# Performance work log

Measured on AMD Instinct MI355X. Metric: run time of the kernel, lower is better.

## Reference

```python
import jax, jax.numpy as jnp
import numpy as np

HEADS = 2
BN_EPS = 1e-5


def _axial_self_attn(x, Wq, Wkv, Wout, bout):
    # x: (b, s, t, c) -- attend along t (the axial sequence dim)
    b, s, t, c = x.shape
    dh = c // HEADS
    q = (x @ Wq).reshape(b, s, t, HEADS, dh)
    k, v = jnp.split(x @ Wkv, 2, axis=-1)  # matches torch .chunk(2, dim=-1)
    k = k.reshape(b, s, t, HEADS, dh)
    v = v.reshape(b, s, t, HEADS, dh)
    dots = jnp.einsum('bsind,bsjnd->bsnij', q, k) * (dh ** -0.5)
    attn = jax.nn.softmax(dots, axis=-1)
    out = jnp.einsum('bsnij,bsjnd->bsind', attn, v).reshape(b, s, t, c)
    return out @ Wout + bout


def setup_inputs() -> dict:
    key = jax.random.key(0)
    ks = jax.random.split(key, 8)
    B, C, H, W = 8, 128, 256, 256
    E = 2 * C
    sd = 0.05
    return {
        'x': jax.random.normal(ks[0], (B, C, H, W), jnp.float32),
        'Wq_h': jax.random.normal(ks[1], (C, C), jnp.float32) * sd,
        'Wkv_h': jax.random.normal(ks[2], (C, 2 * C), jnp.float32) * sd,
        'Wout_h': jax.random.normal(ks[3], (C, C), jnp.float32) * sd,
        'bout_h': jnp.zeros((C,), jnp.float32),
        'Wq_w': jax.random.normal(ks[4], (C, C), jnp.float32) * sd,
        'Wkv_w': jax.random.normal(ks[5], (C, 2 * C), jnp.float32) * sd,
        'Wout_w': jax.random.normal(ks[6], (C, C), jnp.float32) * sd,
        'bout_w': jnp.zeros((C,), jnp.float32),
        'conv_w': jax.random.normal(ks[7], (E, E), jnp.float32) * sd,  # (in, out); torch conv weight[o,i,0,0].T
        'gamma': jnp.ones((E,), jnp.float32),
        'beta': jnp.zeros((E,), jnp.float32),
    }


def reference(x, Wq_h, Wkv_h, Wout_h, bout_h, Wq_w, Wkv_w, Wout_w, bout_w, conv_w, gamma, beta):
    B, C, H, W = x.shape
    # MaxPool2d(2)
    xp = x.reshape(B, C, H // 2, 2, W // 2, 2).max(axis=(3, 5))  # (B,C,H2,W2)
    xc = jnp.transpose(xp, (0, 2, 3, 1))  # (B,H2,W2,C) channels-last
    # AxialAttention, sum_axial_out=True: height-axis attn + width-axis attn
    a_h = _axial_self_attn(jnp.transpose(xc, (0, 2, 1, 3)), Wq_h, Wkv_h, Wout_h, bout_h)
    a_h = jnp.transpose(a_h, (0, 2, 1, 3))
    a_w = _axial_self_attn(xc, Wq_w, Wkv_w, Wout_w, bout_w)
    a = jax.nn.relu(a_h + a_w)
    # cat((x_attn, x), dim=channel) then conv1x1 -> relu -> BatchNorm (batch stats)
    y = jnp.concatenate([a, xc], axis=-1) @ conv_w  # (B,H2,W2,2C)
    y = jax.nn.relu(y)
    mean = y.mean(axis=(0, 1, 2))
    var = y.var(axis=(0, 1, 2))
    y = (y - mean) * jax.lax.rsqrt(var + BN_EPS) * gamma + beta
    return jnp.transpose(y, (0, 3, 1, 2))  # back to NCHW
```

## Files before the change

kernel.cpp:

```cpp
#include <hip/hip_runtime.h>


typedef short v8s __attribute__((ext_vector_type(8)));
typedef short v4s __attribute__((ext_vector_type(4)));
typedef float v4f __attribute__((ext_vector_type(4)));

#define LSA 136
#define LSC 264
#define LSP 130

static __device__ __forceinline__ short f2bf(float f){
  unsigned u = __builtin_bit_cast(unsigned, f);
  u = (u + 0x7FFFu + ((u >> 16) & 1u)) >> 16;
  return (short)u;
}
static __device__ __forceinline__ float bf2f(short s){
  unsigned u = ((unsigned)(unsigned short)s) << 16;
  return __builtin_bit_cast(float, u);
}

__global__ void prep_kernel(const float* __restrict__ Wq_h, const float* __restrict__ Wkv_h,
                            const float* __restrict__ Wout_h, const float* __restrict__ Wq_w,
                            const float* __restrict__ Wkv_w, const float* __restrict__ Wout_w,
                            const float* __restrict__ conv_w, short* __restrict__ wt,
                            float* __restrict__ stats){
  int idx = blockIdx.x * 256 + threadIdx.x;
  if (idx < 8192) stats[idx] = 0.0f;
  const float* src; int K, O, base;
  if      (idx <  16384){ base = 0;      K=128; O=128; src=Wq_h;  }
  else if (idx <  49152){ base = 16384;  K=128; O=256; src=Wkv_h; }
  else if (idx <  65536){ base = 49152;  K=128; O=128; src=Wout_h;}
  else if (idx <  81920){ base = 65536;  K=128; O=128; src=Wq_w;  }
  else if (idx < 114688){ base = 81920;  K=128; O=256; src=Wkv_w; }
  else if (idx < 131072){ base = 114688; K=128; O=128; src=Wout_w;}
  else                  { base = 131072; K=256; O=256; src=conv_w;}
  int local = idx - base;
  int o = local / K, i = local - o * K;
  wt[idx] = f2bf(src[i * O + o]);
}

__global__ __launch_bounds__(256, 4)
void pool_kernel(const float* __restrict__ x, short* __restrict__ xph,
                 short* __restrict__ xpw){
  __shared__ short t_[128*LSP];
  int bx = blockIdx.x;
  int b = bx >> 7, i = bx & 127;
  int tid = (int)threadIdx.x;
  int j  = tid & 127;
  int ch = tid >> 7;
  for (int rep = 0; rep < 64; ++rep){
    int c = rep*2 + ch;
    const float* p0 = x + (((b*128 + c)*256 + 2*i)*256 + 2*j);
    float2 a  = *(const float2*)p0;
    float2 bb = *(const float2*)(p0 + 256);
    t_[j*LSP + c] = f2bf(fmaxf(fmaxf(a.x, a.y), fmaxf(bb.x, bb.y)));
  }
  __syncthreads();
  int obase_h = ((b*128 + i)*128)*128;
  for (int rep = 0; rep < 8; ++rep){
    int idx = rep*256 + tid;
    int row = idx >> 4, seg = idx & 15;
    v8s v = *(const v8s*)(&t_[row*LSP + seg*8]);
    *(v8s*)(xph + obase_h + row*128 + seg*8) = v;
    *(v8s*)(xpw + ((b*128 + row)*128 + i)*128 + seg*8) = v;
  }
}

__global__ __launch_bounds__(512, 2)
void attn_kernel(const short* __restrict__ xp_hw, const short* __restrict__ xp_wh,
                 const short* __restrict__ wt,
                 const float* __restrict__ bout_h, const float* __restrict__ bout_w,
                 short* __restrict__ ah, short* __restrict__ aw){
  __shared__ short A[128*LSA];
  __shared__ short WB[128*LSA];

  const int bx = blockIdx.x;
  const int dir = bx & 1;
  const int sb = bx >> 1;
  const int b = sb >> 7, s = sb & 127;
  const int tid = (int)threadIdx.x;
  const int w = tid >> 6;
  const int lane = tid & 63;
  const int l15 = lane & 15, l4 = lane >> 4;

  const short* Wq   = wt + dir*65536;
  const short* Wk   = Wq + 16384;
  const short* Wv   = Wq + 32768;
  const short* Wout = Wq + 49152;
  const float* bsrc = dir ? bout_w : bout_h;
  const short* xsrc = dir ? xp_hw : xp_wh;
  short*       ao   = dir ? aw : ah;

  const int xbase = ((b*128 + s)*128 + (16*w + l15))*128;
  v8s av[4];
  #pragma unroll
  for (int kk = 0; kk < 4; ++kk)
    av[kk] = *(const v8s*)(xsrc + xbase + kk*32 + l4*8);
  v8s wq_r[4], wk_r[4], wv_r[4], wo_r[4];
  #pragma unroll
  for (int r = 0; r < 4; ++r){
    int idx = (r*512 + tid) * 8;
    wq_r[r] = *(const v8s*)(Wq   + idx);
    wk_r[r] = *(const v8s*)(Wk   + idx);
    wv_r[r] = *(const v8s*)(Wv   + idx);
    wo_r[r] = *(const v8s*)(Wout + idx);
  }

#define STAGE_R(RG)                                                      \
  { _Pragma("unroll")                                                    \
    for (int r_ = 0; r_ < 4; ++r_){                                      \
      int idx_ = (r_*512 + tid) * 8;                                     \
      int oc_ = idx_ >> 7, ic_ = idx_ & 127;                             \
      *(v8s*)(&WB[oc_*LSA + ic_]) = RG[r_];                              \
    } }

  STAGE_R(wq_r);
  __syncthreads();

  #pragma unroll
  for (int tc = 0; tc < 8; ++tc){
    v4f d = {0.f,0.f,0.f,0.f};
    #pragma unroll
    for (int kk = 0; kk < 4; ++kk){
      v8s bf = *(const v8s*)(&WB[(tc*16 + l15)*LSA + kk*32 + l4*8]);
      d = __builtin_amdgcn_mfma_f32_16x16x32_bf16(av[kk], bf, d, 0, 0, 0);
    }
    #pragma unroll
    for (int r = 0; r < 4; ++r)
      A[(16*w + 4*l4 + r)*LSA + 16*tc + l15] = f2bf(d[r]);
  }
  v8s bq[2][2];
  #pragma unroll
  for (int h = 0; h < 2; ++h)
    #pragma unroll
    for (int kk = 0; kk < 2; ++kk)
      bq[h][kk] = *(const v8s*)(&A[(16*w + l15)*LSA + h*64 + kk*32 + l4*8]);
  __syncthreads();

  STAGE_R(wk_r);
  __syncthreads();

  #pragma unroll
  for (int tc = 0; tc < 8; ++tc){
    v4f d = {0.f,0.f,0.f,0.f};
    #pragma unroll
    for (int kk = 0; kk < 4; ++kk){
      v8s bf = *(const v8s*)(&WB[(tc*16 + l15)*LSA + kk*32 + l4*8]);
      d = __builtin_amdgcn_mfma_f32_16x16x32_bf16(av[kk], bf, d, 0, 0, 0);
    }
    #pragma unroll
    for (int r = 0; r < 4; ++r)
      A[(16*w + 4*l4 + r)*LSA + 16*tc + l15] = f2bf(d[r]);
  }
  __syncthreads();

  STAGE_R(wv_r);

  v4s pk[2][8];
  #pragma unroll
  for (int h = 0; h < 2; ++h){
    v4f st[8];
    #pragma unroll
    for (int jt = 0; jt < 8; ++jt){
      v4f d = {0.f,0.f,0.f,0.f};
      #pragma unroll
      for (int kk = 0; kk < 2; ++kk){
        v8s ak = *(const v8s*)(&A[(16*jt + l15)*LSA + h*64 + kk*32 + l4*8]);
        d = __builtin_amdgcn_mfma_f32_16x16x32_bf16(ak, bq[h][kk], d, 0, 0, 0);
      }
      st[jt] = d;
    }
    float mx = -1e30f;
    #pragma unroll
    for (int jt = 0; jt < 8; ++jt)
      #pragma unroll
      for (int r = 0; r < 4; ++r) mx = fmaxf(mx, st[jt][r]);
    mx = fmaxf(mx, __shfl_xor(mx, 16));
    mx = fmaxf(mx, __shfl_xor(mx, 32));
    float sm = 0.f;
    #pragma unroll
    for (int jt = 0; jt < 8; ++jt)
      #pragma unroll
      for (int r = 0; r < 4; ++r){
        float e = __expf((st[jt][r] - mx) * 0.125f);
        st[jt][r] = e; sm += e;
      }
    sm += __shfl_xor(sm, 16);
    sm += __shfl_xor(sm, 32);
    float inv = 1.0f / sm;
    #pragma unroll
    for (int jt = 0; jt < 8; ++jt)
      #pragma unroll
      for (int r = 0; r < 4; ++r) pk[h][jt][r] = f2bf(st[jt][r] * inv);
  }
  __syncthreads();

  v8s pa[2][4];
  #pragma unroll
  for (int h = 0; h < 2; ++h){
    #pragma unroll
    for (int jt = 0; jt < 8; ++jt)
      *(v4s*)(&A[(16*w + l15)*LSA + 16*jt + 4*l4]) = pk[h][jt];
    #pragma unroll
    for (int kk = 0; kk < 4; ++kk)
      pa[h][kk] = *(const v8s*)(&A[(16*w + l15)*LSA + kk*32 + l4*8]);
  }
  __syncthreads();

  #pragma unroll
  for (int tc = 0; tc < 8; ++tc){
    v4f d = {0.f,0.f,0.f,0.f};
    #pragma unroll
    for (int kk = 0; kk < 4; ++kk){
      v8s bf = *(const v8s*)(&WB[(tc*16 + l15)*LSA + kk*32 + l4*8]);
      d = __builtin_amdgcn_mfma_f32_16x16x32_bf16(av[kk], bf, d, 0, 0, 0);
    }
    v4s pkv;
    #pragma unroll
    for (int r = 0; r < 4; ++r) pkv[r] = f2bf(d[r]);
    *(v4s*)(&A[(16*tc + l15)*LSA + 16*w + 4*l4]) = pkv;
  }
  __syncthreads();

  STAGE_R(wo_r);

  v4f ot[2][4];
  #pragma unroll
  for (int h = 0; h < 2; ++h)
    #pragma unroll
    for (int tc = 0; tc < 4; ++tc){
      v4f d = {0.f,0.f,0.f,0.f};
      #pragma unroll
      for (int kk = 0; kk < 4; ++kk){
        v8s vf = *(const v8s*)(&A[(64*h + 16*tc + l15)*LSA + kk*32 + l4*8]);
        d = __builtin_amdgcn_mfma_f32_16x16x32_bf16(vf, pa[h][kk], d, 0, 0, 0);
      }
      ot[h][tc] = d;
    }
  __syncthreads();

  #pragma unroll
  for (int h = 0; h < 2; ++h)
    #pragma unroll
    for (int tc = 0; tc < 4; ++tc){
      v4s pko;
      #pragma unroll
      for (int r = 0; r < 4; ++r) pko[r] = f2bf(ot[h][tc][r]);
      *(v4s*)(&A[(16*w + l15)*LSA + 64*h + 16*tc + 4*l4]) = pko;
    }
  v8s ob[4];
  #pragma unroll
  for (int kk = 0; kk < 4; ++kk)
    ob[kk] = *(const v8s*)(&A[(16*w + l15)*LSA + kk*32 + l4*8]);
  #pragma unroll
  for (int tc = 0; tc < 8; ++tc){
    v4f d = {0.f,0.f,0.f,0.f};
    #pragma unroll
    for (int kk = 0; kk < 4; ++kk){
      v8s awf = *(const v8s*)(&WB[(tc*16 + l15)*LSA + kk*32 + l4*8]);
      d = __builtin_amdgcn_mfma_f32_16x16x32_bf16(awf, ob[kk], d, 0, 0, 0);
    }
    v4f bias = *(const v4f*)(bsrc + 16*tc + 4*l4);
    v4s z;
    #pragma unroll
    for (int r = 0; r < 4; ++r) z[r] = f2bf(d[r] + bias[r]);
    *(v4s*)(&A[(16*w + l15)*LSA + 16*tc + 4*l4]) = z;
  }
  __syncthreads();

  int obase = ((b*128 + s)*128)*128;
  #pragma unroll
  for (int r = 0; r < 4; ++r){
    int idx = (r*512 + tid) * 8;
    int t = idx >> 7, c = idx & 127;
    *(v8s*)(ao + obase + t*128 + c) = *(const v8s*)(&A[t*LSA + c]);
  }
#undef STAGE_R
}

__global__ __launch_bounds__(512, 2)
void conv_kernel(const short* __restrict__ ah, const short* __restrict__ aw,
                 const short* __restrict__ xp, const short* __restrict__ wt,
                 short* __restrict__ yb, float* __restrict__ stats){
  __shared__ short cats[128*LSC];
  __shared__ float lsum[256];
  __shared__ float lsq[256];
  const short* convT = wt + 131072;
  int bx = blockIdx.x;
  int b = bx >> 7, ii = bx & 127;
  int tid = (int)threadIdx.x;
  int wv = tid >> 6, lane = tid & 63, l15 = lane & 15, l4 = lane >> 4;
  if (tid < 256){ lsum[tid] = 0.f; lsq[tid] = 0.f; }

  v8s wf[2][8];
  #pragma unroll
  for (int x = 0; x < 2; ++x)
    #pragma unroll
    for (int kk = 0; kk < 8; ++kk)
      wf[x][kk] = *(const v8s*)(convT + (((wv + 8*x)*16 + l15)*256) + kk*32 + l4*8);

  for (int r = 0; r < 4; ++r){
    int idx = (r*512 + tid) * 8;
    int t = idx >> 7, c = idx & 127;
    v8s hv = *(const v8s*)(ah + ((b*128 + t)*128 + ii)*128 + c);
    v8s wv_ = *(const v8s*)(aw + ((b*128 + ii)*128 + t)*128 + c);
    v8s o;
    #pragma unroll
    for (int k = 0; k < 8; ++k)
      o[k] = f2bf(fmaxf(bf2f(hv[k]) + bf2f(wv_[k]), 0.f));
    *(v8s*)(&cats[t*LSC + c]) = o;
    *(v8s*)(&cats[t*LSC + 128 + c]) =
        *(const v8s*)(xp + ((b*128 + ii)*128 + t)*128 + c);
  }
  __syncthreads();

  v4s ypk[2][8];
  float s1[2] = {0.f,0.f}, s2[2] = {0.f,0.f};
  #pragma unroll
  for (int tt = 0; tt < 8; ++tt){
    v4f d0 = {0.f,0.f,0.f,0.f}, d1 = {0.f,0.f,0.f,0.f};
    #pragma unroll
    for (int kk = 0; kk < 8; ++kk){
      v8s af = *(const v8s*)(&cats[(16*tt + l15)*LSC + kk*32 + l4*8]);
      d0 = __builtin_amdgcn_mfma_f32_16x16x32_bf16(af, wf[0][kk], d0, 0, 0, 0);
      d1 = __builtin_amdgcn_mfma_f32_16x16x32_bf16(af, wf[1][kk], d1, 0, 0, 0);
    }
    #pragma unroll
    for (int r = 0; r < 4; ++r){
      float y0 = fmaxf(d0[r], 0.f), y1 = fmaxf(d1[r], 0.f);
      ypk[0][tt][r] = f2bf(y0); ypk[1][tt][r] = f2bf(y1);
      s1[0] += y0; s2[0] += y0*y0;
      s1[1] += y1; s2[1] += y1*y1;
    }
  }
  #pragma unroll
  for (int x = 0; x < 2; ++x){
    s1[x] += __shfl_xor(s1[x], 16); s1[x] += __shfl_xor(s1[x], 32);
    s2[x] += __shfl_xor(s2[x], 16); s2[x] += __shfl_xor(s2[x], 32);
  }
  if (l4 == 0){
    #pragma unroll
    for (int x = 0; x < 2; ++x){
      int e = (wv + 8*x)*16 + l15;
      atomicAdd(&lsum[e], s1[x]);
      atomicAdd(&lsq[e],  s2[x]);
    }
  }
  __syncthreads();
  #pragma unroll
  for (int x = 0; x < 2; ++x)
    #pragma unroll
    for (int tt = 0; tt < 8; ++tt)
      *(v4s*)(&cats[((wv + 8*x)*16 + l15)*132 + 16*tt + 4*l4]) = ypk[x][tt];
  __syncthreads();
  for (int r = 0; r < 8; ++r){
    int idx = (r*512 + tid) * 8;
    int e = idx >> 7, j = idx & 127;
    *(v8s*)(yb + ((b*256 + e)*128 + ii)*128 + j) = *(const v8s*)(&cats[e*132 + j]);
  }
  if (tid < 256){
    int c = bx & 15;
    atomicAdd(&stats[c*512 + tid],       lsum[tid]);
    atomicAdd(&stats[c*512 + 256 + tid], lsq[tid]);
  }
}

__global__ void bn_kernel(const short* __restrict__ yb, float* __restrict__ out,
                          const float* __restrict__ stats,
                          const float* __restrict__ gamma, const float* __restrict__ beta){
  const float invn = 1.0f / 131072.0f;
  int bx = blockIdx.x;
  int e = bx & 255;
  float s1 = 0.f, s2 = 0.f;
  #pragma unroll
  for (int c = 0; c < 16; ++c){
    s1 += stats[c*512 + e];
    s2 += stats[c*512 + 256 + e];
  }
  float m   = s1 * invn;
  float var = s2 * invn - m * m;
  float sc  = gamma[e] * rsqrtf(var + 1e-5f);
  float sh  = beta[e] - m * sc;
  int base = bx * 16384;
  int tid = (int)threadIdx.x;
  for (int rep = 0; rep < 8; ++rep){
    int idx = base + (rep*256 + tid)*8;
    v8s yv = *(const v8s*)(yb + idx);
    v4f o1, o2;
    #pragma unroll
    for (int r = 0; r < 4; ++r){
      o1[r] = bf2f(yv[r])   * sc + sh;
      o2[r] = bf2f(yv[4+r]) * sc + sh;
    }
    *(v4f*)(out + idx)     = o1;
    *(v4f*)(out + idx + 4) = o2;
  }
}

extern "C" void kernel_launch(void* const* d_in, const int* in_sizes, int n_in,
                              void* d_out, int out_size, void* d_ws, size_t ws_size,
                              hipStream_t stream){
  const float* x      = (const float*)d_in[0];
  const float* Wq_h   = (const float*)d_in[1];
  const float* Wkv_h  = (const float*)d_in[2];
  const float* Wout_h = (const float*)d_in[3];
  const float* bout_h = (const float*)d_in[4];
  const float* Wq_w   = (const float*)d_in[5];
  const float* Wkv_w  = (const float*)d_in[6];
  const float* Wout_w = (const float*)d_in[7];
  const float* bout_w = (const float*)d_in[8];
  const float* conv_w = (const float*)d_in[9];
  const float* gamma  = (const float*)d_in[10];
  const float* beta   = (const float*)d_in[11];
  float* out = (float*)d_out;

  char* ws = (char*)d_ws;
  short* xp_hw = (short*)(ws);
  short* xp_wh = (short*)(ws +  33554432);
  short* ah    = (short*)(ws +  67108864);
  short* aw    = (short*)(ws + 100663296);
  short* yb    = (short*)(ws + 134217728);
  short* wt    = (short*)(ws + 201326592);
  float* stats = (float*)(ws + 201719808);

  prep_kernel<<<768, 256, 0, stream>>>(Wq_h, Wkv_h, Wout_h, Wq_w, Wkv_w, Wout_w,
                                       conv_w, wt, stats);
  pool_kernel<<<1024, 256, 0, stream>>>(x, xp_hw, xp_wh);
  attn_kernel<<<2048, 512, 0, stream>>>(xp_hw, xp_wh, wt, bout_h, bout_w, ah, aw);
  conv_kernel<<<1024, 512, 0, stream>>>(ah, aw, xp_hw, wt, yb, stats);
  bn_kernel<<<2048, 256, 0, stream>>>(yb, out, stats, gamma, beta);
}
```

Baseline: 283.4 us.

## Cut attention kernel register pressure and vectorize pooling loads

The pooling kernel now reads four floats per load, producing two pooled outputs per thread, so it issues fewer, wider global loads. The attention kernel stops holding all four weight matrices in registers and loads each one directly from global memory into LDS just before it is used. The projection GEMMs are re-tiled so each wave computes a 32-row by 64-column block instead of 16 rows by 128 columns. Together with launch bounds raised from 2 to 4 blocks per CU, this aims to lower register use and raise occupancy. The cost is that weight-load latency is now exposed at each staging step rather than prefetched.

```diff
diff --git a/kernel.cpp b/kernel.cpp
--- a/kernel.cpp
+++ b/kernel.cpp
@@ -4,6 +4,7 @@
 typedef short v8s __attribute__((ext_vector_type(8)));
 typedef short v4s __attribute__((ext_vector_type(4)));
 typedef float v4f __attribute__((ext_vector_type(4)));
+typedef float v4flt __attribute__((ext_vector_type(4)));
 
 #define LSA 136
 #define LSC 264
@@ -46,14 +47,15 @@
   int bx = blockIdx.x;
   int b = bx >> 7, i = bx & 127;
   int tid = (int)threadIdx.x;
-  int j  = tid & 127;
-  int ch = tid >> 7;
-  for (int rep = 0; rep < 64; ++rep){
-    int c = rep*2 + ch;
-    const float* p0 = x + (((b*128 + c)*256 + 2*i)*256 + 2*j);
-    float2 a  = *(const float2*)p0;
-    float2 bb = *(const float2*)(p0 + 256);
-    t_[j*LSP + c] = f2bf(fmaxf(fmaxf(a.x, a.y), fmaxf(bb.x, bb.y)));
+  int j2 = tid & 63;
+  int cq = tid >> 6;
+  for (int rep = 0; rep < 32; ++rep){
+    int c = cq*32 + rep;
+    const float* p0 = x + (((b*128 + c)*256 + 2*i)*256 + 4*j2);
+    v4flt a  = *(const v4flt*)p0;
+    v4flt bb = *(const v4flt*)(p0 + 256);
+    t_[(2*j2)*LSP + c]   = f2bf(fmaxf(fmaxf(a[0], a[1]), fmaxf(bb[0], bb[1])));
+    t_[(2*j2+1)*LSP + c] = f2bf(fmaxf(fmaxf(a[2], a[3]), fmaxf(bb[2], bb[3])));
   }
   __syncthreads();
   int obase_h = ((b*128 + i)*128)*128;
@@ -66,7 +68,7 @@
   }
 }
 
-__global__ __launch_bounds__(512, 2)
+__global__ __launch_bounds__(512, 4)
 void attn_kernel(const short* __restrict__ xp_hw, const short* __restrict__ xp_wh,
                  const short* __restrict__ wt,
                  const float* __restrict__ bout_h, const float* __restrict__ bout_w,
@@ -80,6 +82,8 @@
   const int b = sb >> 7, s = sb & 127;
   const int tid = (int)threadIdx.x;
   const int w = tid >> 6;
+  const int m = w >> 1;
+  const int p = w & 1;
   const int lane = tid & 63;
   const int l15 = lane & 15, l4 = lane >> 4;
 
@@ -91,70 +95,59 @@
   const short* xsrc = dir ? xp_hw : xp_wh;
   short*       ao   = dir ? aw : ah;
 
-  const int xbase = ((b*128 + s)*128 + (16*w + l15))*128;
-  v8s av[4];
-  #pragma unroll
-  for (int kk = 0; kk < 4; ++kk)
-    av[kk] = *(const v8s*)(xsrc + xbase + kk*32 + l4*8);
-  v8s wq_r[4], wk_r[4], wv_r[4], wo_r[4];
-  #pragma unroll
-  for (int r = 0; r < 4; ++r){
-    int idx = (r*512 + tid) * 8;
-    wq_r[r] = *(const v8s*)(Wq   + idx);
-    wk_r[r] = *(const v8s*)(Wk   + idx);
-    wv_r[r] = *(const v8s*)(Wv   + idx);
-    wo_r[r] = *(const v8s*)(Wout + idx);
-  }
-
-#define STAGE_R(RG)                                                      \
+  v8s av[2][4];
+  #pragma unroll
+  for (int ti = 0; ti < 2; ++ti){
+    int xbase = ((b*128 + s)*128 + (32*m + 16*ti + l15))*128;
+    #pragma unroll
+    for (int kk = 0; kk < 4; ++kk)
+      av[ti][kk] = *(const v8s*)(xsrc + xbase + kk*32 + l4*8);
+  }
+
+#define STAGE_W(SRC)                                                     \
   { _Pragma("unroll")                                                    \
     for (int r_ = 0; r_ < 4; ++r_){                                      \
       int idx_ = (r_*512 + tid) * 8;                                     \
       int oc_ = idx_ >> 7, ic_ = idx_ & 127;                             \
-      *(v8s*)(&WB[oc_*LSA + ic_]) = RG[r_];                              \
+      *(v8s*)(&WB[oc_*LSA + ic_]) = *(const v8s*)((SRC) + idx_);         \
     } }
 
-  STAGE_R(wq_r);
-  __syncthreads();
-
-  #pragma unroll
-  for (int tc = 0; tc < 8; ++tc){
-    v4f d = {0.f,0.f,0.f,0.f};
-    #pragma unroll
-    for (int kk = 0; kk < 4; ++kk){
-      v8s bf = *(const v8s*)(&WB[(tc*16 + l15)*LSA + kk*32 + l4*8]);
-      d = __builtin_amdgcn_mfma_f32_16x16x32_bf16(av[kk], bf, d, 0, 0, 0);
-    }
-    #pragma unroll
-    for (int r = 0; r < 4; ++r)
-      A[(16*w + 4*l4 + r)*LSA + 16*tc + l15] = f2bf(d[r]);
-  }
+#define WGEMM_TO_A()                                                     \
+  { _Pragma("unroll")                                                    \
+    for (int ti = 0; ti < 2; ++ti){                                      \
+      _Pragma("unroll")                                                  \
+      for (int tc = 0; tc < 4; ++tc){                                    \
+        int ocb = 64*p + 16*tc;                                          \
+        v4f d = {0.f,0.f,0.f,0.f};                                       \
+        _Pragma("unroll")                                                \
+        for (int kk = 0; kk < 4; ++kk){                                  \
+          v8s bf = *(const v8s*)(&WB[(ocb + l15)*LSA + kk*32 + l4*8]);   \
+          d = __builtin_amdgcn_mfma_f32_16x16x32_bf16(av[ti][kk], bf, d, 0, 0, 0); \
+        }                                                                \
+        _Pragma("unroll")                                                \
+        for (int r = 0; r < 4; ++r)                                      \
+          A[(32*m + 16*ti + 4*l4 + r)*LSA + ocb + l15] = f2bf(d[r]);     \
+      } } }
+
+  STAGE_W(Wq);
+  __syncthreads();
+
+  WGEMM_TO_A();
+  __syncthreads();
+
   v8s bq[2][2];
   #pragma unroll
   for (int h = 0; h < 2; ++h)
     #pragma unroll
     for (int kk = 0; kk < 2; ++kk)
       bq[h][kk] = *(const v8s*)(&A[(16*w + l15)*LSA + h*64 + kk*32 + l4*8]);
-  __syncthreads();
-
-  STAGE_R(wk_r);
-  __syncthreads();
-
-  #pragma unroll
-  for (int tc = 0; tc < 8; ++tc){
-    v4f d = {0.f,0.f,0.f,0.f};
-    #pragma unroll
-    for (int kk = 0; kk < 4; ++kk){
-      v8s bf = *(const v8s*)(&WB[(tc*16 + l15)*LSA + kk*32 + l4*8]);
-      d = __builtin_amdgcn_mfma_f32_16x16x32_bf16(av[kk], bf, d, 0, 0, 0);
-    }
-    #pragma unroll
-    for (int r = 0; r < 4; ++r)
-      A[(16*w + 4*l4 + r)*LSA + 16*tc + l15] = f2bf(d[r]);
-  }
-  __syncthreads();
-
-  STAGE_R(wv_r);
+  STAGE_W(Wk);
+  __syncthreads();
+
+  WGEMM_TO_A();
+  __syncthreads();
+
+  STAGE_W(Wv);
 
   v4s pk[2][8];
   #pragma unroll
@@ -208,21 +201,25 @@
   __syncthreads();
 
   #pragma unroll
-  for (int tc = 0; tc < 8; ++tc){
-    v4f d = {0.f,0.f,0.f,0.f};
-    #pragma unroll
-    for (int kk = 0; kk < 4; ++kk){
-      v8s bf = *(const v8s*)(&WB[(tc*16 + l15)*LSA + kk*32 + l4*8]);
-      d = __builtin_amdgcn_mfma_f32_16x16x32_bf16(av[kk], bf, d, 0, 0, 0);
-    }
-    v4s pkv;
-    #pragma unroll
-    for (int r = 0; r < 4; ++r) pkv[r] = f2bf(d[r]);
-    *(v4s*)(&A[(16*tc + l15)*LSA + 16*w + 4*l4]) = pkv;
-  }
-  __syncthreads();
-
-  STAGE_R(wo_r);
+  for (int ti = 0; ti < 2; ++ti){
+    #pragma unroll
+    for (int tc = 0; tc < 4; ++tc){
+      int ocb = 64*p + 16*tc;
+      v4f d = {0.f,0.f,0.f,0.f};
+      #pragma unroll
+      for (int kk = 0; kk < 4; ++kk){
+        v8s bf = *(const v8s*)(&WB[(ocb + l15)*LSA + kk*32 + l4*8]);
+        d = __builtin_amdgcn_mfma_f32_16x16x32_bf16(av[ti][kk], bf, d, 0, 0, 0);
+      }
+      v4s pkv;
+      #pragma unroll
+      for (int r = 0; r < 4; ++r) pkv[r] = f2bf(d[r]);
+      *(v4s*)(&A[(ocb + l15)*LSA + 32*m + 16*ti + 4*l4]) = pkv;
+    }
+  }
+  __syncthreads();
+
+  STAGE_W(Wout);
 
   v4f ot[2][4];
   #pragma unroll
@@ -275,7 +272,8 @@
     int t = idx >> 7, c = idx & 127;
     *(v8s*)(ao + obase + t*128 + c) = *(const v8s*)(&A[t*LSA + c]);
   }
-#undef STAGE_R
+#undef STAGE_W
+#undef WGEMM_TO_A
 }
 
 __global__ __launch_bounds__(512, 2)
```

Result: slower. 304.2 us (+7.4%).

## Process two axial slices per attention block sharing staged weights; widen pool loads

Applied to the files above, without the earlier changes.

The attention kernel now runs 1024-thread blocks that handle two slices at once, each half using its own activation buffer in LDS. The weight tiles are staged into shared memory once per block and used by both slices, which halves the weight staging per slice. Weights are now copied straight from global memory to LDS rather than being prefetched into registers, which lowers register pressure but exposes that load latency before each barrier. The pool kernel also switches to 16-byte loads, each producing two pooled outputs, and changes how channels are assigned to threads. The launch bounds ask for four 1024-thread blocks per CU, which the LDS footprint likely cannot support.

```diff
diff --git a/kernel.cpp b/kernel.cpp
--- a/kernel.cpp
+++ b/kernel.cpp
@@ -4,6 +4,7 @@
 typedef short v8s __attribute__((ext_vector_type(8)));
 typedef short v4s __attribute__((ext_vector_type(4)));
 typedef float v4f __attribute__((ext_vector_type(4)));
+typedef float v4flt __attribute__((ext_vector_type(4)));
 
 #define LSA 136
 #define LSC 264
@@ -46,14 +47,15 @@
   int bx = blockIdx.x;
   int b = bx >> 7, i = bx & 127;
   int tid = (int)threadIdx.x;
-  int j  = tid & 127;
-  int ch = tid >> 7;
-  for (int rep = 0; rep < 64; ++rep){
-    int c = rep*2 + ch;
-    const float* p0 = x + (((b*128 + c)*256 + 2*i)*256 + 2*j);
-    float2 a  = *(const float2*)p0;
-    float2 bb = *(const float2*)(p0 + 256);
-    t_[j*LSP + c] = f2bf(fmaxf(fmaxf(a.x, a.y), fmaxf(bb.x, bb.y)));
+  int j2 = tid & 63;
+  int cq = tid >> 6;
+  for (int rep = 0; rep < 32; ++rep){
+    int c = cq*32 + rep;
+    const float* p0 = x + (((b*128 + c)*256 + 2*i)*256 + 4*j2);
+    v4flt a  = *(const v4flt*)p0;
+    v4flt bb = *(const v4flt*)(p0 + 256);
+    t_[(2*j2)*LSP + c]   = f2bf(fmaxf(fmaxf(a[0], a[1]), fmaxf(bb[0], bb[1])));
+    t_[(2*j2+1)*LSP + c] = f2bf(fmaxf(fmaxf(a[2], a[3]), fmaxf(bb[2], bb[3])));
   }
   __syncthreads();
   int obase_h = ((b*128 + i)*128)*128;
@@ -66,22 +68,27 @@
   }
 }
 
-__global__ __launch_bounds__(512, 2)
+__global__ __launch_bounds__(1024, 4)
 void attn_kernel(const short* __restrict__ xp_hw, const short* __restrict__ xp_wh,
                  const short* __restrict__ wt,
                  const float* __restrict__ bout_h, const float* __restrict__ bout_w,
                  short* __restrict__ ah, short* __restrict__ aw){
-  __shared__ short A[128*LSA];
+  __shared__ short A2[2][128*LSA];
   __shared__ short WB[128*LSA];
 
   const int bx = blockIdx.x;
   const int dir = bx & 1;
   const int sb = bx >> 1;
-  const int b = sb >> 7, s = sb & 127;
+  const int b = sb >> 6, sp = sb & 63;
   const int tid = (int)threadIdx.x;
-  const int w = tid >> 6;
+  const int prob = tid >> 9;
+  const int ptid = tid & 511;
+  const int w = ptid >> 6;
   const int lane = tid & 63;
   const int l15 = lane & 15, l4 = lane >> 4;
+  const int s = sp*2 + prob;
+
+  short* A = &A2[prob][0];
 
   const short* Wq   = wt + dir*65536;
   const short* Wk   = Wq + 16384;
@@ -91,30 +98,22 @@
   const short* xsrc = dir ? xp_hw : xp_wh;
   short*       ao   = dir ? aw : ah;
 
-  const int xbase = ((b*128 + s)*128 + (16*w + l15))*128;
+  const int trow = 16*w + l15;
+  const int xbase = ((b*128 + s)*128 + trow)*128;
   v8s av[4];
   #pragma unroll
   for (int kk = 0; kk < 4; ++kk)
     av[kk] = *(const v8s*)(xsrc + xbase + kk*32 + l4*8);
-  v8s wq_r[4], wk_r[4], wv_r[4], wo_r[4];
-  #pragma unroll
-  for (int r = 0; r < 4; ++r){
-    int idx = (r*512 + tid) * 8;
-    wq_r[r] = *(const v8s*)(Wq   + idx);
-    wk_r[r] = *(const v8s*)(Wk   + idx);
-    wv_r[r] = *(const v8s*)(Wv   + idx);
-    wo_r[r] = *(const v8s*)(Wout + idx);
-  }
-
-#define STAGE_R(RG)                                                      \
+
+#define STAGE_W(SRC)                                                     \
   { _Pragma("unroll")                                                    \
-    for (int r_ = 0; r_ < 4; ++r_){                                      \
-      int idx_ = (r_*512 + tid) * 8;                                     \
+    for (int r_ = 0; r_ < 2; ++r_){                                      \
+      int idx_ = (r_*1024 + tid) * 8;                                    \
       int oc_ = idx_ >> 7, ic_ = idx_ & 127;                             \
-      *(v8s*)(&WB[oc_*LSA + ic_]) = RG[r_];                              \
+      *(v8s*)(&WB[oc_*LSA + ic_]) = *(const v8s*)((SRC) + idx_);         \
     } }
 
-  STAGE_R(wq_r);
+  STAGE_W(Wq);
   __syncthreads();
 
   #pragma unroll
@@ -137,7 +136,7 @@
       bq[h][kk] = *(const v8s*)(&A[(16*w + l15)*LSA + h*64 + kk*32 + l4*8]);
   __syncthreads();
 
-  STAGE_R(wk_r);
+  STAGE_W(Wk);
   __syncthreads();
 
   #pragma unroll
@@ -154,7 +153,7 @@
   }
   __syncthreads();
 
-  STAGE_R(wv_r);
+  STAGE_W(Wv);
 
   v4s pk[2][8];
   #pragma unroll
@@ -222,7 +221,7 @@
   }
   __syncthreads();
 
-  STAGE_R(wo_r);
+  STAGE_W(Wout);
 
   v4f ot[2][4];
   #pragma unroll
@@ -271,11 +270,11 @@
   int obase = ((b*128 + s)*128)*128;
   #pragma unroll
   for (int r = 0; r < 4; ++r){
-    int idx = (r*512 + tid) * 8;
+    int idx = (r*512 + ptid) * 8;
     int t = idx >> 7, c = idx & 127;
     *(v8s*)(ao + obase + t*128 + c) = *(const v8s*)(&A[t*LSA + c]);
   }
-#undef STAGE_R
+#undef STAGE_W
 }
 
 __global__ __launch_bounds__(512, 2)
@@ -426,7 +425,7 @@
   prep_kernel<<<768, 256, 0, stream>>>(Wq_h, Wkv_h, Wout_h, Wq_w, Wkv_w, Wout_w,
                                        conv_w, wt, stats);
   pool_kernel<<<1024, 256, 0, stream>>>(x, xp_hw, xp_wh);
-  attn_kernel<<<2048, 512, 0, stream>>>(xp_hw, xp_wh, wt, bout_h, bout_w, ah, aw);
+  attn_kernel<<<1024, 1024, 0, stream>>>(xp_hw, xp_wh, wt, bout_h, bout_w, ah, aw);
   conv_kernel<<<1024, 512, 0, stream>>>(ah, aw, xp_hw, wt, yb, stats);
   bn_kernel<<<2048, 256, 0, stream>>>(yb, out, stats, gamma, beta);
 }
```

New measurement: 285.5 us. No clear change (+0.7%).

## Drop transposed pooled copy and widen pool loads to float4

Applied to the files above, without the earlier changes.

The pool kernel now writes a single bf16 channels-last pooled tensor instead of two copies, one of them transposed. The attention kernel reads the height-direction rows from that one tensor with strided addressing, where each row is 256 bytes apart by 128*128 elements. Each thread in the pool kernel also loads float4 values and produces two pooled outputs, so it issues fewer, wider loads. This removes one 32 MB write, but the height-direction attention loads become scattered 256-byte rows instead of contiguous ones.

```diff
diff --git a/kernel.cpp b/kernel.cpp
--- a/kernel.cpp
+++ b/kernel.cpp
@@ -4,6 +4,7 @@
 typedef short v8s __attribute__((ext_vector_type(8)));
 typedef short v4s __attribute__((ext_vector_type(4)));
 typedef float v4f __attribute__((ext_vector_type(4)));
+typedef float v4flt __attribute__((ext_vector_type(4)));
 
 #define LSA 136
 #define LSC 264
@@ -40,35 +41,32 @@
 }
 
 __global__ __launch_bounds__(256, 4)
-void pool_kernel(const float* __restrict__ x, short* __restrict__ xph,
-                 short* __restrict__ xpw){
+void pool_kernel(const float* __restrict__ x, short* __restrict__ xp){
   __shared__ short t_[128*LSP];
   int bx = blockIdx.x;
   int b = bx >> 7, i = bx & 127;
   int tid = (int)threadIdx.x;
-  int j  = tid & 127;
-  int ch = tid >> 7;
-  for (int rep = 0; rep < 64; ++rep){
-    int c = rep*2 + ch;
-    const float* p0 = x + (((b*128 + c)*256 + 2*i)*256 + 2*j);
-    float2 a  = *(const float2*)p0;
-    float2 bb = *(const float2*)(p0 + 256);
-    t_[j*LSP + c] = f2bf(fmaxf(fmaxf(a.x, a.y), fmaxf(bb.x, bb.y)));
-  }
-  __syncthreads();
-  int obase_h = ((b*128 + i)*128)*128;
+  int j2 = tid & 63;
+  int cq = tid >> 6;
+  for (int rep = 0; rep < 32; ++rep){
+    int c = cq*32 + rep;
+    const float* p0 = x + (((b*128 + c)*256 + 2*i)*256 + 4*j2);
+    v4flt a  = *(const v4flt*)p0;
+    v4flt bb = *(const v4flt*)(p0 + 256);
+    t_[(2*j2)*LSP + c]   = f2bf(fmaxf(fmaxf(a[0], a[1]), fmaxf(bb[0], bb[1])));
+    t_[(2*j2+1)*LSP + c] = f2bf(fmaxf(fmaxf(a[2], a[3]), fmaxf(bb[2], bb[3])));
+  }
+  __syncthreads();
+  int obase = ((b*128 + i)*128)*128;
   for (int rep = 0; rep < 8; ++rep){
     int idx = rep*256 + tid;
     int row = idx >> 4, seg = idx & 15;
-    v8s v = *(const v8s*)(&t_[row*LSP + seg*8]);
-    *(v8s*)(xph + obase_h + row*128 + seg*8) = v;
-    *(v8s*)(xpw + ((b*128 + row)*128 + i)*128 + seg*8) = v;
+    *(v8s*)(xp + obase + row*128 + seg*8) = *(const v8s*)(&t_[row*LSP + seg*8]);
   }
 }
 
 __global__ __launch_bounds__(512, 2)
-void attn_kernel(const short* __restrict__ xp_hw, const short* __restrict__ xp_wh,
-                 const short* __restrict__ wt,
+void attn_kernel(const short* __restrict__ xp, const short* __restrict__ wt,
                  const float* __restrict__ bout_h, const float* __restrict__ bout_w,
                  short* __restrict__ ah, short* __restrict__ aw){
   __shared__ short A[128*LSA];
@@ -88,14 +86,15 @@
   const short* Wv   = Wq + 32768;
   const short* Wout = Wq + 49152;
   const float* bsrc = dir ? bout_w : bout_h;
-  const short* xsrc = dir ? xp_hw : xp_wh;
   short*       ao   = dir ? aw : ah;
 
-  const int xbase = ((b*128 + s)*128 + (16*w + l15))*128;
+  const int trow = 16*w + l15;
+  const int xbase = dir ? (((b*128 + s)*128 + trow)*128)
+                        : (((b*128 + trow)*128 + s)*128);
   v8s av[4];
   #pragma unroll
   for (int kk = 0; kk < 4; ++kk)
-    av[kk] = *(const v8s*)(xsrc + xbase + kk*32 + l4*8);
+    av[kk] = *(const v8s*)(xp + xbase + kk*32 + l4*8);
   v8s wq_r[4], wk_r[4], wv_r[4], wo_r[4];
   #pragma unroll
   for (int r = 0; r < 4; ++r){
@@ -415,18 +414,17 @@
   float* out = (float*)d_out;
 
   char* ws = (char*)d_ws;
-  short* xp_hw = (short*)(ws);
-  short* xp_wh = (short*)(ws +  33554432);
-  short* ah    = (short*)(ws +  67108864);
-  short* aw    = (short*)(ws + 100663296);
-  short* yb    = (short*)(ws + 134217728);
-  short* wt    = (short*)(ws + 201326592);
-  float* stats = (float*)(ws + 201719808);
+  short* xp    = (short*)(ws);
+  short* ah    = (short*)(ws +  33554432);
+  short* aw    = (short*)(ws +  67108864);
+  short* yb    = (short*)(ws + 100663296);
+  short* wt    = (short*)(ws + 167772160);
+  float* stats = (float*)(ws + 168165376);
 
   prep_kernel<<<768, 256, 0, stream>>>(Wq_h, Wkv_h, Wout_h, Wq_w, Wkv_w, Wout_w,
                                        conv_w, wt, stats);
-  pool_kernel<<<1024, 256, 0, stream>>>(x, xp_hw, xp_wh);
-  attn_kernel<<<2048, 512, 0, stream>>>(xp_hw, xp_wh, wt, bout_h, bout_w, ah, aw);
-  conv_kernel<<<1024, 512, 0, stream>>>(ah, aw, xp_hw, wt, yb, stats);
+  pool_kernel<<<1024, 256, 0, stream>>>(x, xp);
+  attn_kernel<<<2048, 512, 0, stream>>>(xp, wt, bout_h, bout_w, ah, aw);
+  conv_kernel<<<1024, 512, 0, stream>>>(ah, aw, xp, wt, yb, stats);
   bn_kernel<<<2048, 256, 0, stream>>>(yb, out, stats, gamma, beta);
 }
```

Result: no change. 287.4 us (+1.4%).
